# Kernel tuning notes

Measured on AMD Instinct MI355X. Metric: run time of the kernel, lower is better.

## Reference

```python
import jax, jax.numpy as jnp
import numpy as np

LOW_THRESH, HIGH_THRESH = 0.1, 0.2   # kornia canny defaults
HYST_ITERS = 10                      # fixed-point hysteresis iterations (fixed for jit)


def _gaussian_kernel5(sigma=1.0):
    x = jnp.arange(5, dtype=jnp.float32) - 2.0
    g = jnp.exp(-0.5 * (x / sigma) ** 2)
    g = g / g.sum()
    return jnp.outer(g, g)  # [5,5]


def _conv2d(x, k):
    # x: [B,1,H,W]; k: [kh,kw]; reflect pad + VALID conv == SAME with reflect border
    kh, kw = k.shape
    xp = jnp.pad(x, ((0, 0), (0, 0), (kh // 2, kh // 2), (kw // 2, kw // 2)), mode="reflect")
    return jax.lax.conv_general_dilated(
        xp, k[None, None], (1, 1), "VALID",
        dimension_numbers=("NCHW", "OIHW", "NCHW"))


def _shift(x, dy, dx):
    # value of neighbor at (i+dy, j+dx), zero-padded border; x: [B,1,H,W]
    H, W = x.shape[2], x.shape[3]
    xp = jnp.pad(x, ((0, 0), (0, 0), (1, 1), (1, 1)))
    return xp[:, :, 1 + dy:1 + dy + H, 1 + dx:1 + dx + W]


def _canny_edges(img):
    # img: [B,3,H,W] in [0,1] -> binary edge map [B,1,H,W]
    gray = 0.299 * img[:, :1] + 0.587 * img[:, 1:2] + 0.114 * img[:, 2:3]
    blur = _conv2d(gray, _gaussian_kernel5())
    sobel_x = jnp.array([[-1., 0., 1.], [-2., 0., 2.], [-1., 0., 1.]], jnp.float32)
    gx = _conv2d(blur, sobel_x)
    gy = _conv2d(blur, sobel_x.T)
    mag = jnp.sqrt(gx * gx + gy * gy + 1e-12)
    ang = jnp.arctan2(gy, gx)

    # non-maximum suppression: quantize gradient direction to 4 bins (0/45/90/135 deg)
    b = jnp.mod(jnp.round(ang / (jnp.pi / 4.0)), 4).astype(jnp.int32)  # [B,1,H,W]
    n_pos = jnp.stack([_shift(mag, 0, 1), _shift(mag, 1, 1),
                       _shift(mag, 1, 0), _shift(mag, 1, -1)], axis=0)  # [4,B,1,H,W]
    n_neg = jnp.stack([_shift(mag, 0, -1), _shift(mag, -1, -1),
                       _shift(mag, -1, 0), _shift(mag, -1, 1)], axis=0)
    n1 = jnp.take_along_axis(n_pos, b[None], axis=0)[0]
    n2 = jnp.take_along_axis(n_neg, b[None], axis=0)[0]
    nms = jnp.where((mag >= n1) & (mag >= n2), mag, 0.0)

    # double threshold: strong=1.0, weak=0.5
    edges = jnp.where(nms >= HIGH_THRESH, 1.0,
                      jnp.where(nms >= LOW_THRESH, 0.5, 0.0))

    # hysteresis: weak pixels with a strong 8-neighbor become strong (iterated)
    def body(_, e):
        strong = (e == 1.0).astype(e.dtype)
        nb = jax.lax.reduce_window(strong, 0.0, jax.lax.max,
                                   (1, 1, 3, 3), (1, 1, 1, 1), "SAME")
        promoted = (e == 0.5) & (nb > 0.5)
        return jnp.where(promoted, 1.0, e)

    edges = jax.lax.fori_loop(0, HYST_ITERS, body, edges)
    return (edges == 1.0).astype(jnp.float32)


def setup_inputs() -> dict:
    key = jax.random.key(0)
    k1, k2 = jax.random.split(key)
    shape = (16, 3, 512, 512)
    return {"y_hat": jax.random.uniform(k1, shape, jnp.float32),
            "y": jax.random.uniform(k2, shape, jnp.float32)}


def reference(y_hat, y):
    y_hat_edges = _canny_edges(y_hat)
    y_edges = _canny_edges(y)
    return jnp.mean(jnp.abs(y_hat_edges - y_edges))  # F.l1_loss, mean reduction
```

## Files before the change

### kernel.cpp

```cpp
#include <hip/hip_runtime.h>
#include <math.h>

#define H 512
#define W 512
#define IMG (H*W)
#define NIMG 32

typedef unsigned long long u64;

__device__ __forceinline__ int reflect_idx(int i, int n) {
    if (i < 0) i = -i;
    if (i >= n) i = 2 * n - 2 - i;
    return i;
}

#define S0 0.05448868454964294f
#define S1 0.35317871110251920f
#define S2 0.94551131545035710f
#define S3 1.29364257779496160f
#define A1 0.05448868454964294f
#define A2 0.24420134200323332f
#define A3 0.34813126234460456f

#define TY 16

__global__ __launch_bounds__(256) void k_edges(const float* __restrict__ yhat,
                                               const float* __restrict__ yy,
                                               u64* __restrict__ strongP,
                                               u64* __restrict__ weakP) {
    __shared__ __align__(16) char lds[8320 + 14144];
    float (*sg)[80] = (float (*)[80])lds;
    float (*hxy)[68][2] = (float (*)[68][2])(lds + 8320);
    float (*sm)[68] = (float (*)[68])lds;
    unsigned char (*sbin)[68] = (unsigned char (*)[68])(lds + 5440);

    const int n = blockIdx.z;
    const float* src = (n < 16) ? (yhat + (size_t)n * 3 * IMG)
                                : (yy + (size_t)(n - 16) * 3 * IMG);
    const int x0 = blockIdx.x * 64;
    const int y0 = blockIdx.y * TY;
    const int tx = threadIdx.x, ty = threadIdx.y;
    const int tid = ty * 64 + tx;

    if (x0 >= 8 && x0 + 68 <= W) {
        for (int t = tid; t < 26 * 19; t += 256) {
            int sy = t / 19, f = t % 19;
            int iy = reflect_idx(y0 - 4 + sy, H);
            const float4* rp = (const float4*)(src + (size_t)iy * W + (x0 - 8));
            float4 r = rp[f];
            float4 g = rp[f + IMG / 4];
            float4 b = rp[f + 2 * (IMG / 4)];
            float4 gr;
            gr.x = 0.299f * r.x + 0.587f * g.x + 0.114f * b.x;
            gr.y = 0.299f * r.y + 0.587f * g.y + 0.114f * b.y;
            gr.z = 0.299f * r.z + 0.587f * g.z + 0.114f * b.z;
            gr.w = 0.299f * r.w + 0.587f * g.w + 0.114f * b.w;
            *(float4*)&sg[sy][4 * f] = gr;
        }
    } else {
        for (int t = tid; t < 26 * 76; t += 256) {
            int sy = t / 76, c = t % 76;
            int iy = reflect_idx(y0 - 4 + sy, H);
            int ix = reflect_idx(x0 - 8 + c, W);
            const float* row = src + (size_t)iy * W;
            float r = row[ix], g = row[IMG + ix], b = row[2 * IMG + ix];
            sg[sy][c] = 0.299f * r + 0.587f * g + 0.114f * b;
        }
    }
    __syncthreads();

    for (int t = tid; t < 26 * 17; t += 256) {
        int sy = t / 17, g = t % 17;
        const float4* p = (const float4*)&sg[sy][0];
        float4 q0 = p[g + 1], q1 = p[g + 2], q2 = p[g + 3];
        float w[12] = {q0.x, q0.y, q0.z, q0.w, q1.x, q1.y, q1.z, q1.w,
                       q2.x, q2.y, q2.z, q2.w};
#pragma unroll
        for (int j = 0; j < 4; j++) {
            float hx = A3 * (w[j + 4] - w[j + 2]) + A2 * (w[j + 5] - w[j + 1])
                     + A1 * (w[j + 6] - w[j + 0]);
            float hy = S3 * w[j + 3] + S2 * (w[j + 4] + w[j + 2])
                     + S1 * (w[j + 5] + w[j + 1]) + S0 * (w[j + 6] + w[j + 0]);
            *(float2*)&hxy[sy][4 * g + j][0] = make_float2(hx, hy);
        }
    }
    __syncthreads();

    for (int t = tid; t < 5 * 66; t += 256) {
        int rg = t / 66, c = t % 66;
        float hx[10], hy[10];
#pragma unroll
        for (int i = 0; i < 10; i++) {
            float2 v = *(const float2*)&hxy[4 * rg + i][c][0];
            hx[i] = v.x; hy[i] = v.y;
        }
        int imgcol = x0 - 1 + c;
        bool colok = (unsigned)imgcol < (unsigned)W;
#pragma unroll
        for (int j = 0; j < 4; j++) {
            int my = 4 * rg + j;
            float gx = S3 * hx[j + 3] + S2 * (hx[j + 4] + hx[j + 2])
                     + S1 * (hx[j + 5] + hx[j + 1]) + S0 * (hx[j + 6] + hx[j + 0]);
            float gy = A3 * (hy[j + 4] - hy[j + 2]) + A2 * (hy[j + 5] - hy[j + 1])
                     + A1 * (hy[j + 6] - hy[j + 0]);
            int imgrow = y0 - 1 + my;
            bool ok = colok && ((unsigned)imgrow < (unsigned)H);
            float m2 = ok ? (gx * gx + gy * gy + 1e-12f) : 0.f;
            sm[my][c] = m2;
            float ax = fabsf(gx), ay = fabsf(gy);
            int d;
            if (ay <= 0.4142135623730951f * ax) d = 1;
            else if (ay >= 2.414213562373095f * ax) d = 68;
            else d = ((gx > 0.f) == (gy > 0.f)) ? 69 : 67;
            sbin[my][c] = (unsigned char)d;
        }
    }
    __syncthreads();

#pragma unroll
    for (int k = 0; k < 4; k++) {
        int ry = ty + 4 * k;
        const float* cp = &sm[ry + 1][tx + 1];
        float mag = cp[0];
        int d = sbin[ry + 1][tx + 1];
        float n1 = cp[d];
        float n2 = cp[-d];
        float nms = (mag >= n1 && mag >= n2) ? mag : 0.f;
        u64 strong = __ballot(nms >= 0.04f);
        u64 weak = __ballot(nms >= 0.01f);
        if (tx == 0) {
            size_t off = ((size_t)n * 8 + blockIdx.x) * H + (y0 + ry);
            strongP[off] = strong;
            weakP[off] = weak;
        }
    }
}

__device__ __forceinline__ u64 ldw(const u64* p, int img, int y, int w, bool ok) {
    return (ok && w >= 0 && w < 8) ? p[((size_t)img * 8 + w) * H + y] : 0ULL;
}

__global__ __launch_bounds__(256) void k_hyst(const u64* __restrict__ strongP,
                                              const u64* __restrict__ weakP,
                                              unsigned int* __restrict__ partials) {
    __shared__ unsigned int part[4];
    const int wy = threadIdx.x >> 6;
    const int wave = blockIdx.x * 4 + wy;
    const int lane = threadIdx.x & 63;
    const int tile = wave & 255;
    const int pair = wave >> 8;
    const int tx0 = (tile & 15) * 32;
    const int ty0 = (tile >> 4) * 32;

    const int y = ty0 - 10 + lane;
    const bool rowok = (lane < 52) && (y >= 0) && (y < H);
    const int yc = rowok ? y : 0;
    const int s = tx0 - 10;
    const int w0i = s >> 6;
    const int r = s & 63;

    const int imgA = pair, imgB = pair + 16;
    u64 sA, wA, sB, wB;
    {
        u64 lo, hi;
        lo = ldw(strongP, imgA, yc, w0i, rowok); hi = ldw(strongP, imgA, yc, w0i + 1, rowok);
        sA = (lo >> r) | (hi << (64 - r));
        lo = ldw(weakP, imgA, yc, w0i, rowok);   hi = ldw(weakP, imgA, yc, w0i + 1, rowok);
        wA = (lo >> r) | (hi << (64 - r));
        lo = ldw(strongP, imgB, yc, w0i, rowok); hi = ldw(strongP, imgB, yc, w0i + 1, rowok);
        sB = (lo >> r) | (hi << (64 - r));
        lo = ldw(weakP, imgB, yc, w0i, rowok);   hi = ldw(weakP, imgB, yc, w0i + 1, rowok);
        wB = (lo >> r) | (hi << (64 - r));
    }

#pragma unroll
    for (int it = 0; it < 10; it++) {
        u64 up = __shfl_up(sA, 1), dn = __shfl_down(sA, 1);
        u64 t = up | sA | dn;
        sA |= (t | (t << 1) | (t >> 1)) & wA;
        up = __shfl_up(sB, 1); dn = __shfl_down(sB, 1);
        t = up | sB | dn;
        sB |= (t | (t << 1) | (t >> 1)) & wB;
    }

    unsigned int c = 0;
    if (lane >= 10 && lane < 42) {
        const u64 mask = ((1ULL << 42) - (1ULL << 10));
        c = (unsigned int)__popcll((sA ^ sB) & mask);
    }
#pragma unroll
    for (int off = 32; off > 0; off >>= 1) c += __shfl_down(c, off);
    if (lane == 0) part[wy] = c;
    __syncthreads();
    if (threadIdx.x == 0)
        partials[blockIdx.x] = part[0] + part[1] + part[2] + part[3];
}

__global__ __launch_bounds__(256) void k_final(const unsigned int* __restrict__ partials,
                                               float* __restrict__ out) {
    __shared__ unsigned int part[4];
    unsigned int c = 0;
    for (int i = threadIdx.x; i < 1024; i += 256) c += partials[i];
#pragma unroll
    for (int off = 32; off > 0; off >>= 1) c += __shfl_down(c, off);
    const int lane = threadIdx.x & 63;
    const int wy = threadIdx.x >> 6;
    if (lane == 0) part[wy] = c;
    __syncthreads();
    if (threadIdx.x == 0)
        out[0] = (float)(part[0] + part[1] + part[2] + part[3]) * (1.0f / 4194304.0f);
}

extern "C" void kernel_launch(void* const* d_in, const int* in_sizes, int n_in,
                              void* d_out, int out_size, void* d_ws, size_t ws_size,
                              hipStream_t stream) {
    const float* yhat = (const float*)d_in[0];
    const float* yy = (const float*)d_in[1];

    u64* strongP = (u64*)d_ws;
    u64* weakP = strongP + (size_t)NIMG * H * 8;
    unsigned int* partials = (unsigned int*)(weakP + (size_t)NIMG * H * 8);

    dim3 eblk(64, 4);
    dim3 egrd(W / 64, H / TY, NIMG);
    k_edges<<<egrd, eblk, 0, stream>>>(yhat, yy, strongP, weakP);

    k_hyst<<<1024, 256, 0, stream>>>(strongP, weakP, partials);
    k_final<<<1, 256, 0, stream>>>(partials, (float*)d_out);
}
```

Measured before the change: 146.7 us.

## Enlarge edge-kernel row tile to 48 rows with 512-thread blocks

```diff
diff --git a/kernel.cpp b/kernel.cpp
--- a/kernel.cpp
+++ b/kernel.cpp
@@ -22,17 +22,19 @@
 #define A2 0.24420134200323332f
 #define A3 0.34813126234460456f
 
-#define TY 16
-
-__global__ __launch_bounds__(256) void k_edges(const float* __restrict__ yhat,
+#define TY 48
+#define SGROWS 58
+#define SMROWS 52
+
+__global__ __launch_bounds__(512) void k_edges(const float* __restrict__ yhat,
                                                const float* __restrict__ yy,
                                                u64* __restrict__ strongP,
                                                u64* __restrict__ weakP) {
-    __shared__ __align__(16) char lds[8320 + 14144];
+    __shared__ __align__(16) char lds[18560 + 31552];
     float (*sg)[80] = (float (*)[80])lds;
-    float (*hxy)[68][2] = (float (*)[68][2])(lds + 8320);
+    float (*hxy)[68][2] = (float (*)[68][2])(lds + 18560);
     float (*sm)[68] = (float (*)[68])lds;
-    unsigned char (*sbin)[68] = (unsigned char (*)[68])(lds + 5440);
+    unsigned char (*sbin)[68] = (unsigned char (*)[68])(lds + 14144);
 
     const int n = blockIdx.z;
     const float* src = (n < 16) ? (yhat + (size_t)n * 3 * IMG)
@@ -42,34 +44,37 @@
     const int tx = threadIdx.x, ty = threadIdx.y;
     const int tid = ty * 64 + tx;
 
-    if (x0 >= 8 && x0 + 68 <= W) {
-        for (int t = tid; t < 26 * 19; t += 256) {
-            int sy = t / 19, f = t % 19;
-            int iy = reflect_idx(y0 - 4 + sy, H);
-            const float4* rp = (const float4*)(src + (size_t)iy * W + (x0 - 8));
-            float4 r = rp[f];
-            float4 g = rp[f + IMG / 4];
-            float4 b = rp[f + 2 * (IMG / 4)];
-            float4 gr;
+    const int xb = x0 - 8;
+    for (int t = tid; t < SGROWS * 19; t += 512) {
+        int sy = t / 19, f = t % 19;
+        int iy = reflect_idx(y0 - 4 + sy, H);
+        const float* row = src + (size_t)iy * W;
+        int c0 = xb + 4 * f;
+        float4 gr;
+        if (c0 >= 0 && c0 + 3 < W) {
+            const float4* rp = (const float4*)(row + c0);
+            float4 r = rp[0];
+            float4 g = rp[IMG / 4];
+            float4 b = rp[2 * (IMG / 4)];
             gr.x = 0.299f * r.x + 0.587f * g.x + 0.114f * b.x;
             gr.y = 0.299f * r.y + 0.587f * g.y + 0.114f * b.y;
             gr.z = 0.299f * r.z + 0.587f * g.z + 0.114f * b.z;
             gr.w = 0.299f * r.w + 0.587f * g.w + 0.114f * b.w;
-            *(float4*)&sg[sy][4 * f] = gr;
-        }
-    } else {
-        for (int t = tid; t < 26 * 76; t += 256) {
-            int sy = t / 76, c = t % 76;
-            int iy = reflect_idx(y0 - 4 + sy, H);
-            int ix = reflect_idx(x0 - 8 + c, W);
-            const float* row = src + (size_t)iy * W;
-            float r = row[ix], g = row[IMG + ix], b = row[2 * IMG + ix];
-            sg[sy][c] = 0.299f * r + 0.587f * g + 0.114f * b;
-        }
-    }
-    __syncthreads();
-
-    for (int t = tid; t < 26 * 17; t += 256) {
+        } else {
+            float v[4];
+#pragma unroll
+            for (int j = 0; j < 4; j++) {
+                int ix = reflect_idx(c0 + j, W);
+                v[j] = 0.299f * row[ix] + 0.587f * row[IMG + ix]
+                     + 0.114f * row[2 * IMG + ix];
+            }
+            gr.x = v[0]; gr.y = v[1]; gr.z = v[2]; gr.w = v[3];
+        }
+        *(float4*)&sg[sy][4 * f] = gr;
+    }
+    __syncthreads();
+
+    for (int t = tid; t < SGROWS * 17; t += 512) {
         int sy = t / 17, g = t % 17;
         const float4* p = (const float4*)&sg[sy][0];
         float4 q0 = p[g + 1], q1 = p[g + 2], q2 = p[g + 3];
@@ -86,7 +91,7 @@
     }
     __syncthreads();
 
-    for (int t = tid; t < 5 * 66; t += 256) {
+    for (int t = tid; t < 13 * 66; t += 512) {
         int rg = t / 66, c = t % 66;
         float hx[10], hy[10];
 #pragma unroll
@@ -118,8 +123,8 @@
     __syncthreads();
 
 #pragma unroll
-    for (int k = 0; k < 4; k++) {
-        int ry = ty + 4 * k;
+    for (int k = 0; k < 6; k++) {
+        int ry = ty + 8 * k;
         const float* cp = &sm[ry + 1][tx + 1];
         float mag = cp[0];
         int d = sbin[ry + 1][tx + 1];
@@ -128,7 +133,7 @@
         float nms = (mag >= n1 && mag >= n2) ? mag : 0.f;
         u64 strong = __ballot(nms >= 0.04f);
         u64 weak = __ballot(nms >= 0.01f);
-        if (tx == 0) {
+        if (tx == 0 && (y0 + ry) < H) {
             size_t off = ((size_t)n * 8 + blockIdx.x) * H + (y0 + ry);
             strongP[off] = strong;
             weakP[off] = weak;
@@ -221,8 +226,8 @@
     u64* weakP = strongP + (size_t)NIMG * H * 8;
     unsigned int* partials = (unsigned int*)(weakP + (size_t)NIMG * H * 8);
 
-    dim3 eblk(64, 4);
-    dim3 egrd(W / 64, H / TY, NIMG);
+    dim3 eblk(64, 8);
+    dim3 egrd(W / 64, (H + TY - 1) / TY, NIMG);
     k_edges<<<egrd, eblk, 0, stream>>>(yhat, yy, strongP, weakP);
 
     k_hyst<<<1024, 256, 0, stream>>>(strongP, weakP, partials);
```

After: 153.8 us. +4.9%, slower.
